# Performance work log

Hardware: AMD Instinct MI355X
Metric: run time of the kernel (lower is better)

## Reference

```python
import jax, jax.numpy as jnp
import numpy as np


def _gru(x, h, Wih, Whh, bih, bhh):
    # PyTorch GRU cell: gates ordered (reset, update, new)
    gi = x @ Wih + bih
    gh = h @ Whh + bhh
    ir, iz, inew = jnp.split(gi, 3, -1)
    hr, hz, hn = jnp.split(gh, 3, -1)
    r = jax.nn.sigmoid(ir + hr)
    u = jax.nn.sigmoid(iz + hz)
    n = jnp.tanh(inew + r * hn)
    return (1.0 - u) * n + u * h


def _kld_e(m1, s1, m2, s2):
    # elementwise term of kld_gauss (before the 0.5 * sum)
    return 2.0 * jnp.log(s2) - 2.0 * jnp.log(s1) + (s1 * s1 + (m1 - m2) ** 2) / (s2 * s2) - 1.0


def setup_inputs() -> dict:
    T, B, F, H, Z, G, A, NN, C = 32, 512, 512, 512, 256, 3, 10, 3, 1000
    key = jax.random.key(0)
    ks = iter(jax.random.split(key, 64))
    def rn(shape):
        return jax.random.normal(next(ks), shape, jnp.float32)
    def W(shape):
        return rn(shape) * (1.0 / float(np.sqrt(shape[0])))
    z = lambda n: jnp.zeros((n,), jnp.float32)
    return {
        'feat_seq': rn((T, B, F)),
        'h0': rn((B, H)),
        'eps_z': rn((T, B, Z)),
        'eps_goal': rn((G, B, Z)),
        'eps_next': rn((G, A, B, H)),
        'eps_future': rn((NN - 1, A, B, H)),
        'Wpx': W((F, H)), 'bpx': z(H),
        'Wenc1': W((2 * H, H)), 'benc1': z(H), 'Wenc2': W((H, Z)), 'benc2': z(Z),
        'Wpr1': W((H, H)), 'bpr1': z(H), 'Wpr2': W((H, Z)), 'bpr2': z(Z),
        'Wpz': W((Z, H)), 'bpz': z(H),
        'Wih1': W((2 * H, 3 * H)), 'Whh1': W((H, 3 * H)), 'bih1': z(3 * H), 'bhh1': z(3 * H),
        'Wzn': W((Z, H)), 'bzn': z(H),
        'Wprn1': W((H, H)), 'bprn1': z(H), 'Wprn2': W((H, Z)), 'bprn2': z(Z),
        'Wga': W((Z + H, H)), 'bga': z(H),
        'Woa1': W((H, H)), 'boa1': z(H), 'Woa2': W((H, Z)), 'boa2': z(Z),
        'Wna1': W((H, H)), 'bna1': z(H), 'Wna2': W((H, Z)), 'bna2': z(Z),
        'Wen': W((2 * Z, Z)), 'ben': z(Z),
        'Wact': W((H, H)), 'bact': z(H),
        'Wih2': W((2 * H, 3 * H)), 'Whh2': W((H, 3 * H)), 'bih2': z(3 * H), 'bhh2': z(3 * H),
        'Wcc': W((H, C)), 'bcc': z(C),
        'Wnc': W((H, C)), 'bnc': z(C),
    }


def reference(feat_seq, h0, eps_z, eps_goal, eps_next, eps_future,
              Wpx, bpx, Wenc1, benc1, Wenc2, benc2, Wpr1, bpr1, Wpr2, bpr2, Wpz, bpz,
              Wih1, Whh1, bih1, bhh1, Wzn, bzn, Wprn1, bprn1, Wprn2, bprn2, Wga, bga,
              Woa1, boa1, Woa2, boa2, Wna1, bna1, Wna2, bna2, Wen, ben, Wact, bact,
              Wih2, Whh2, bih2, bhh2, Wcc, bcc, Wnc, bnc):
    relu, sp = jax.nn.relu, jax.nn.softplus
    mlp2 = lambda x, W1, b1, W2, b2: relu(x @ W1 + b1) @ W2 + b2
    phi_prior = lambda x: mlp2(x, Wpr1, bpr1, Wpr2, bpr2)
    phi_prior_new = lambda x: mlp2(x, Wprn1, bprn1, Wprn2, bprn2)
    phi_next_act = lambda x: mlp2(x, Wna1, bna1, Wna2, bna2)
    phi_obs_act = lambda x: mlp2(x, Woa1, boa1, Woa2, boa2)
    phi_get_act = lambda x: relu(x @ Wga + bga)
    phi_enc_next = lambda x: relu(x @ Wen + ben)
    phi_act = lambda x: relu(x @ Wact + bact)
    G = eps_goal.shape[0]

    phix = relu(feat_seq @ Wpx + bpx)  # [T,B,H]

    def step(carry, inp):
        h, k = carry
        xp, eps = inp
        enc = mlp2(jnp.concatenate([h, xp], -1), Wenc1, benc1, Wenc2, benc2)  # enc_mean_t
        estd = sp(enc)
        pri = phi_prior(h)
        pstd = sp(pri)
        k = k + 0.5 * jnp.sum(_kld_e(enc, estd, pri, pstd))
        zt = eps * estd + enc  # reparameterized sample
        h = _gru(jnp.concatenate([xp, relu(zt @ Wpz + bpz)], -1), h, Wih1, Whh1, bih1, bhh1)
        return (h, k), None

    (h, kld_lat_goal), _ = jax.lax.scan(step, (h0, jnp.float32(0.0)), (phix, eps_z))

    obs_mean = phi_prior(h)  # [B,Z]
    obs_std = sp(obs_mean)
    obs_goal = obs_mean + eps_goal * obs_std  # [G,B,Z]
    pn_h = jnp.broadcast_to(phi_prior_new(h), (G,) + obs_mean.shape)  # [G,B,Z]
    obs_act = phi_get_act(jnp.concatenate([relu(obs_goal @ Wzn + bzn), pn_h], -1))  # [G,B,H]
    next_mean = phi_get_act(jnp.concatenate([pn_h, obs_act], -1))  # [G,B,H]
    next_std = sp(next_mean)
    next_act = next_mean[:, None] + eps_next * next_std[:, None]  # [G,A,B,H]
    pnext = phi_next_act(next_act)  # [G,A,B,Z] = prior_next_lat_goal_mean
    pnext_std = sp(pnext)
    obs_act_z = phi_obs_act(obs_act)[:, None]  # [G,1,B,Z]
    enc_next = phi_enc_next(jnp.concatenate([pnext, jnp.broadcast_to(obs_act_z, pnext.shape)], -1))
    enc_std = sp(enc_next)
    sym = 0.5 * (jnp.sum(_kld_e(obs_mean, obs_std, enc_next, enc_std), axis=(-1, -2))
                 + jnp.sum(_kld_e(enc_next, enc_std, obs_mean, obs_std), axis=(-1, -2)))  # [G,A]

    # The torch loop's `if i == 0 or ...` resets the running min for every goal
    # candidate, so only the LAST goal candidate's argmin over A survives.
    j = jnp.argmin(sym[G - 1])
    lat_goal_dis = sym[G - 1, j]
    kld_next = 0.5 * jnp.sum(_kld_e(enc_next[G - 1, j], enc_std[G - 1, j], pnext[G - 1, j], pnext_std[G - 1, j]))
    next_act_final = next_act[G - 1, j]  # [B,H]
    obs_act_final = obs_act[G - 1]       # [B,H]

    pre, cur, ha = obs_act_final, next_act_final, h
    kld_future = jnp.float32(0.0)
    future_dis = jnp.float32(0.0)
    future_finals = []
    for i in range(eps_future.shape[0]):  # next_num - 1 sequential steps
        ha = _gru(jnp.concatenate([phi_act(pre), phi_act(cur)], -1), ha, Wih2, Whh2, bih2, bhh2)
        pre = cur
        fmean = phi_get_act(jnp.concatenate([phi_prior_new(ha), pre], -1))  # [B,H]
        fstd = sp(fmean)
        fact = fmean + eps_future[i] * fstd  # [A,B,H]
        pf = phi_next_act(fact)
        pf_std = sp(pf)
        pre_z = jnp.broadcast_to(phi_next_act(pre), pf.shape)
        encf = phi_enc_next(jnp.concatenate([pf, pre_z], -1))
        encf_std = sp(encf)
        symf = 0.5 * (jnp.sum(_kld_e(obs_mean, obs_std, encf, encf_std), axis=(-1, -2))
                      + jnp.sum(_kld_e(encf, encf_std, obs_mean, obs_std), axis=(-1, -2)))  # [A]
        jj = jnp.argmin(symf)
        future_dis = future_dis + symf[jj]
        kld_future = kld_future + 0.5 * jnp.sum(_kld_e(encf[jj], encf_std[jj], pf[jj], pf_std[jj]))
        cur = fact[jj]
        future_finals.append(cur)

    out_next = next_act_final @ Wnc + bnc
    out_future = jnp.stack([out_next] + [f @ Wnc + bnc for f in future_finals], 0)  # [next_num,B,C]
    out_cur = obs_act_final @ Wcc + bcc
    return out_cur, out_future, kld_lat_goal, kld_next, lat_goal_dis, kld_future, future_dis
```

## Files before the change

kernel.cpp:

```cpp
#include <hip/hip_runtime.h>
#include <math.h>

#define DEV __device__ __forceinline__

typedef unsigned short ushort_t;
typedef __attribute__((ext_vector_type(8))) short s8v;
typedef __attribute__((ext_vector_type(4))) float f4v;

DEV float sp_(float x){ float m=fmaxf(x,0.f); return m + log1pf(expf(-fabsf(x))); }
DEV float sig_(float x){ return 1.f/(1.f+expf(-x)); }
DEV float kld_(float m1,float s1,float m2,float s2){
  float d=m1-m2;
  return 2.f*(logf(s2)-logf(s1)) + (s1*s1+d*d)/(s2*s2) - 1.f;
}
DEV unsigned short f2bf(float x){
  unsigned u = __float_as_uint(x);
  u += 0x7FFFu + ((u>>16)&1u);
  return (unsigned short)(u>>16);
}

DEV float blockReduceSum(float v){
  __shared__ float sh[8];
  #pragma unroll
  for(int o=32;o>0;o>>=1) v += __shfl_down(v,o,64);
  int lane = threadIdx.x & 63, wid = threadIdx.x >> 6;
  if(lane==0) sh[wid]=v;
  __syncthreads();
  float r = 0.f;
  if(threadIdx.x < (int)(blockDim.x>>6)) r = sh[threadIdx.x];
  if(wid==0){
    #pragma unroll
    for(int o=4;o>0;o>>=1) r += __shfl_down(r,o,64);
  }
  return r;
}

__global__ __launch_bounds__(256)
void gemm_mf(const float* __restrict__ A1, int lda1, int K1,
             const float* __restrict__ A2, int lda2, int K2,
             const ushort_t* __restrict__ BT, int ldbt,
             const float* __restrict__ bias,
             const float* __restrict__ Cadd, int rowmask, int ldcadd,
             float* __restrict__ Cm, int ldc, int N, int relu_cut)
{
  __shared__ ushort_t As[64][40];
  __shared__ ushort_t Bs[64][40];
  const int tid  = threadIdx.x;
  const int row0 = blockIdx.y * 64;
  const int col0 = blockIdx.x * 64;
  const int lane = tid & 63;
  const int w    = tid >> 6;
  const int wr   = w >> 1, wc = w & 1;
  const int Kt   = K1 + K2;
  f4v acc[2][2];
  #pragma unroll
  for(int i=0;i<2;i++){
    #pragma unroll
    for(int j=0;j<2;j++){ acc[i][j][0]=0.f; acc[i][j][1]=0.f; acc[i][j][2]=0.f; acc[i][j][3]=0.f; }
  }
  const int sr  = tid >> 2;
  const int skc = (tid & 3) * 8;

  for(int k0=0; k0<Kt; k0+=32){
    int kg = k0 + skc;
    const float* ap = (kg < K1) ? (A1 + (size_t)(row0+sr)*lda1 + kg)
                                : (A2 + (size_t)(row0+sr)*lda2 + (kg-K1));
    float4 v0 = *(const float4*)ap;
    float4 v1 = *(const float4*)(ap+4);
    s8v av;
    av[0]=(short)f2bf(v0.x); av[1]=(short)f2bf(v0.y); av[2]=(short)f2bf(v0.z); av[3]=(short)f2bf(v0.w);
    av[4]=(short)f2bf(v1.x); av[5]=(short)f2bf(v1.y); av[6]=(short)f2bf(v1.z); av[7]=(short)f2bf(v1.w);
    *(s8v*)&As[sr][skc] = av;
    int cb = col0 + sr;
    s8v bv = {0,0,0,0,0,0,0,0};
    if(cb < N) bv = *(const s8v*)(BT + (size_t)cb*ldbt + k0 + skc);
    *(s8v*)&Bs[sr][skc] = bv;
    __syncthreads();
    const int fr = lane & 15, fk = (lane >> 4) * 8;
    s8v a0 = *(const s8v*)&As[wr*32      + fr][fk];
    s8v a1 = *(const s8v*)&As[wr*32 + 16 + fr][fk];
    s8v b0 = *(const s8v*)&Bs[wc*32      + fr][fk];
    s8v b1 = *(const s8v*)&Bs[wc*32 + 16 + fr][fk];
    acc[0][0] = __builtin_amdgcn_mfma_f32_16x16x32_bf16(a0,b0,acc[0][0],0,0,0);
    acc[0][1] = __builtin_amdgcn_mfma_f32_16x16x32_bf16(a0,b1,acc[0][1],0,0,0);
    acc[1][0] = __builtin_amdgcn_mfma_f32_16x16x32_bf16(a1,b0,acc[1][0],0,0,0);
    acc[1][1] = __builtin_amdgcn_mfma_f32_16x16x32_bf16(a1,b1,acc[1][1],0,0,0);
    __syncthreads();
  }
  const int fr = lane & 15, fq = lane >> 4;
  #pragma unroll
  for(int fi=0; fi<2; fi++){
    #pragma unroll
    for(int fj=0; fj<2; fj++){
      int col = col0 + wc*32 + fj*16 + fr;
      if(col >= N) continue;
      #pragma unroll
      for(int r=0;r<4;r++){
        int row = row0 + wr*32 + fi*16 + fq*4 + r;
        float v = acc[fi][fj][r];
        if(Cadd) v += Cadd[(size_t)(row & rowmask)*ldcadd + col];
        if(bias) v += bias[col];
        if(col < relu_cut) v = fmaxf(v, 0.f);
        Cm[(size_t)row*ldc + col] = v;
      }
    }
  }
}

template<int BM>
__global__ __launch_bounds__(256)
void gemm_k(const float* __restrict__ A1, int lda1, int K1,
            const float* __restrict__ A2, int lda2, int K2,
            const float* __restrict__ Bm, int ldb,
            const float* __restrict__ bias,
            const float* __restrict__ Cadd, int rowmask, int ldcadd,
            float* __restrict__ Cm, int ldc, int N, int relu_cut)
{
  constexpr int BN = 64, BK = 32;
  constexpr int TM = BM/16;
  constexpr int PAD = (BM>=32) ? 4 : 1;
  __shared__ float As[BK][BM+PAD];
  __shared__ float Bs[BK][BN];
  const int tid = threadIdx.x;
  const int row0 = blockIdx.y * BM;
  const int col0 = blockIdx.x * BN;
  const int tx = tid & 15, ty = tid >> 4;
  float4 acc[TM];
  #pragma unroll
  for(int i=0;i<TM;i++) acc[i] = make_float4(0.f,0.f,0.f,0.f);
  const int Kt = K1 + K2;
  for(int k0=0; k0<Kt; k0+=BK){
    if constexpr (BM>=32){
      #pragma unroll
      for(int j=0;j<BM/32;j++){
        int ci = tid + j*256;
        int r  = ci >> 3;
        int kq = ci & 7;
        int kg = k0 + kq*4;
        const float* ap = (kg < K1) ? (A1 + (size_t)(row0+r)*lda1 + kg)
                                    : (A2 + (size_t)(row0+r)*lda2 + (kg-K1));
        float4 v = *(const float4*)ap;
        As[kq*4+0][r]=v.x; As[kq*4+1][r]=v.y; As[kq*4+2][r]=v.z; As[kq*4+3][r]=v.w;
      }
    } else {
      int r  = tid >> 4;
      int kq = tid & 15;
      int kg = k0 + kq*2;
      const float* ap = (kg < K1) ? (A1 + (size_t)(row0+r)*lda1 + kg)
                                  : (A2 + (size_t)(row0+r)*lda2 + (kg-K1));
      float2 v = *(const float2*)ap;
      As[kq*2+0][r]=v.x; As[kq*2+1][r]=v.y;
    }
    #pragma unroll
    for(int j=0;j<2;j++){
      int ci = tid + j*256;
      int r = ci >> 4, c4 = ci & 15;
      int c = col0 + c4*4;
      float4 v = make_float4(0.f,0.f,0.f,0.f);
      if(c < N) v = *(const float4*)(Bm + (size_t)(k0+r)*ldb + c);
      *(float4*)&Bs[r][c4*4] = v;
    }
    __syncthreads();
    #pragma unroll
    for(int kk=0; kk<BK; kk++){
      float4 b = *(const float4*)&Bs[kk][tx*4];
      if constexpr (TM==4){
        float4 a = *(const float4*)&As[kk][ty*4];
        acc[0].x=fmaf(a.x,b.x,acc[0].x); acc[0].y=fmaf(a.x,b.y,acc[0].y); acc[0].z=fmaf(a.x,b.z,acc[0].z); acc[0].w=fmaf(a.x,b.w,acc[0].w);
        acc[1].x=fmaf(a.y,b.x,acc[1].x); acc[1].y=fmaf(a.y,b.y,acc[1].y); acc[1].z=fmaf(a.y,b.z,acc[1].z); acc[1].w=fmaf(a.y,b.w,acc[1].w);
        acc[2].x=fmaf(a.z,b.x,acc[2].x); acc[2].y=fmaf(a.z,b.y,acc[2].y); acc[2].z=fmaf(a.z,b.z,acc[2].z); acc[2].w=fmaf(a.z,b.w,acc[2].w);
        acc[3].x=fmaf(a.w,b.x,acc[3].x); acc[3].y=fmaf(a.w,b.y,acc[3].y); acc[3].z=fmaf(a.w,b.z,acc[3].z); acc[3].w=fmaf(a.w,b.w,acc[3].w);
      } else if constexpr (TM==2){
        float2 a = *(const float2*)&As[kk][ty*2];
        acc[0].x=fmaf(a.x,b.x,acc[0].x); acc[0].y=fmaf(a.x,b.y,acc[0].y); acc[0].z=fmaf(a.x,b.z,acc[0].z); acc[0].w=fmaf(a.x,b.w,acc[0].w);
        acc[1].x=fmaf(a.y,b.x,acc[1].x); acc[1].y=fmaf(a.y,b.y,acc[1].y); acc[1].z=fmaf(a.y,b.z,acc[1].z); acc[1].w=fmaf(a.y,b.w,acc[1].w);
      } else {
        float a = As[kk][ty];
        acc[0].x=fmaf(a,b.x,acc[0].x); acc[0].y=fmaf(a,b.y,acc[0].y); acc[0].z=fmaf(a,b.z,acc[0].z); acc[0].w=fmaf(a,b.w,acc[0].w);
      }
    }
    __syncthreads();
  }
  int c = col0 + tx*4;
  if(c >= N) return;
  #pragma unroll
  for(int i=0;i<TM;i++){
// ... 124 lines not shown
                      float* __restrict__ h, int B_, int H_){
  int i=blockIdx.x*blockDim.x+threadIdx.x;
  if(i<B_*H_){
    int b=i/H_, c=i%H_;
    const float* gib=gi+(size_t)b*ldgi;
    const float* ghb=gh+(size_t)b*ldgh;
    float r=sig_(gib[c]+ghb[c]);
    float u=sig_(gib[H_+c]+ghb[H_+c]);
    float nn=tanhf(fmaf(r, ghb[2*H_+c], gib[2*H_+c]));
    h[i]=(1.f-u)*nn + u*h[i];
  }
}

extern "C" void kernel_launch(void* const* d_in, const int* in_sizes, int n_in,
                              void* d_out, int out_size, void* d_ws, size_t ws_size,
                              hipStream_t stream)
{
  const int T=32, B=512, F=512, H=512, Z=256, G=3, A=10, C=1000;
  const float* feat   = (const float*)d_in[0];
  const float* h0     = (const float*)d_in[1];
  const float* eps_z  = (const float*)d_in[2];
  const float* eps_g  = (const float*)d_in[3];
  const float* eps_n  = (const float*)d_in[4];
  const float* eps_f  = (const float*)d_in[5];
  const float* Wpx=(const float*)d_in[6],  *bpx=(const float*)d_in[7];
  const float* Wenc1=(const float*)d_in[8],*benc1=(const float*)d_in[9];
  const float* Wenc2=(const float*)d_in[10],*benc2=(const float*)d_in[11];
  const float* Wpr1=(const float*)d_in[12],*bpr1=(const float*)d_in[13];
  const float* Wpr2=(const float*)d_in[14],*bpr2=(const float*)d_in[15];
  const float* Wpz=(const float*)d_in[16], *bpz=(const float*)d_in[17];
  const float* Wih1=(const float*)d_in[18],*Whh1=(const float*)d_in[19];
  const float* bih1=(const float*)d_in[20],*bhh1=(const float*)d_in[21];
  const float* Wzn=(const float*)d_in[22], *bzn=(const float*)d_in[23];
  const float* Wprn1=(const float*)d_in[24],*bprn1=(const float*)d_in[25];
  const float* Wprn2=(const float*)d_in[26],*bprn2=(const float*)d_in[27];
  const float* Wga=(const float*)d_in[28], *bga=(const float*)d_in[29];
  const float* Woa1=(const float*)d_in[30],*boa1=(const float*)d_in[31];
  const float* Woa2=(const float*)d_in[32],*boa2=(const float*)d_in[33];
  const float* Wna1=(const float*)d_in[34],*bna1=(const float*)d_in[35];
  const float* Wna2=(const float*)d_in[36],*bna2=(const float*)d_in[37];
  const float* Wen=(const float*)d_in[38], *ben=(const float*)d_in[39];
  const float* Wact=(const float*)d_in[40],*bact=(const float*)d_in[41];
  const float* Wih2=(const float*)d_in[42],*Whh2=(const float*)d_in[43];
  const float* bih2=(const float*)d_in[44],*bhh2=(const float*)d_in[45];
  const float* Wcc=(const float*)d_in[46], *bcc=(const float*)d_in[47];
  const float* Wnc=(const float*)d_in[48], *bnc=(const float*)d_in[49];

  float* ws = (float*)d_ws;
  size_t off = 0;
  auto alloc = [&](size_t n){ float* p = ws + off; off += n; return p; };
  float* Hb  = alloc((size_t)B*H);
  float* E1  = alloc((size_t)B*H);
  float* P1  = alloc((size_t)B*H);
  float* ZP  = alloc((size_t)B*H);
  float* NM  = alloc((size_t)B*H);
  float* OA  = alloc((size_t)B*H);
  float* PAb = alloc((size_t)B*H);
  float* CAb = alloc((size_t)B*H);
  float* GI  = alloc((size_t)B*3*H);
  float* GH  = alloc((size_t)B*3*H);
  float* ENC = alloc((size_t)B*Z);
  float* PRI = alloc((size_t)B*Z);
  float* ZT  = alloc((size_t)B*Z);
  float* OM  = alloc((size_t)B*Z);
  float* PNH = alloc((size_t)B*Z);
  float* OAZ = alloc((size_t)B*Z);
  float* BASE= alloc((size_t)B*Z);
  float* NACT= alloc((size_t)A*B*H);
  float* PMID= alloc((size_t)A*B*H);
  float* PNX = alloc((size_t)A*B*Z);
  float* ENCN= alloc((size_t)A*B*Z);
  float* BUFA= alloc((size_t)B*H);
  float* BUFB= alloc((size_t)B*H);
  float* BUFC= alloc((size_t)B*H);
  float* C1  = alloc((size_t)B*2560);
  float* C2  = alloc((size_t)B*512);
  float* bb1 = alloc(2560);
  float* bb2 = alloc(512);
  float* SYM = alloc(16);
  float* SYMF0 = alloc(16);
  float* SYMF1 = alloc(16);
  int*   JSEL = (int*)alloc(16);
  size_t mark = off;
  auto ua = [&](size_t n){ ushort_t* p = (ushort_t*)(ws + off); off += n/2; return p; };
  ushort_t* WpxT  = ua((size_t)512*512);
  ushort_t* WB1T  = ua((size_t)2560*1024);
  ushort_t* WB2T  = ua((size_t)512*1024);
  ushort_t* WpzT  = ua((size_t)512*256);
  ushort_t* Wih1T = ua((size_t)1536*1024);
  ushort_t* Wpr1T = ua((size_t)512*512);
  ushort_t* Wpr2T = ua((size_t)256*512);
  ushort_t* Wprn1T= ua((size_t)512*512);
  ushort_t* Wprn2T= ua((size_t)256*512);
  ushort_t* WznT  = ua((size_t)512*256);
  ushort_t* WgaT  = ua((size_t)512*768);
  ushort_t* Woa1T = ua((size_t)512*512);
  ushort_t* Woa2T = ua((size_t)256*512);
  ushort_t* Wna1T = ua((size_t)512*512);
  ushort_t* Wna2T = ua((size_t)256*512);
  ushort_t* WenT  = ua((size_t)256*512);
  ushort_t* WactT = ua((size_t)512*512);
  ushort_t* Wih2T = ua((size_t)1536*1024);
  ushort_t* Whh2T = ua((size_t)1536*512);
  ushort_t* WccT  = ua((size_t)1000*512);
  ushort_t* WncT  = ua((size_t)1000*512);
  bool fast = off*4 <= ws_size;
  if(!fast) off = mark;
  size_t mark2 = off;
  float* PHIX = alloc((size_t)T*B*H);
  bool bigphix = off*4 <= ws_size;
  float* XP = nullptr;
  if(!bigphix){ off = mark2; XP = alloc((size_t)B*H); PHIX = nullptr; }

  float* outCur = (float*)d_out;
  float* outFut = outCur + (size_t)B*C;
  float* S      = outCur + (size_t)B*C*4;

  auto ew = [&](int n){ return dim3((n+255)/256); };
  auto cvt = [&](const float* W, ushort_t* WT, int K, int N){
    k_cvtT<<<(K*N+255)/256,256,0,stream>>>(W,WT,K,N);
  };
  auto mf = [&](const float* A1,int lda1,int K1,
                const float* A2,int lda2,int K2,
                const ushort_t* BT,int ldbt, const float* bias,
                const float* Cadd,int rowmask,int ldcadd,
                float* Cm,int ldc,int M,int N,int cut){
    dim3 g((N+63)/64, M/64);
    gemm_mf<<<g,256,0,stream>>>(A1,lda1,K1, A2?A2:A1,lda2,K2, BT,ldbt,bias,
                                Cadd,rowmask,ldcadd, Cm,ldc,N,cut);
  };
  auto gemm = [&](const float* A1,int lda1,int K1,
                  const float* A2,int lda2,int K2,
                  const float* Bw,int ldb, const float* bias,
                  const float* Cadd,int rowmask,int ldcadd,
                  float* Cm,int ldc,int M,int N,int relu){
    int nb = (N+63)/64;
    int cut = relu ? N : 0;
    if(M%64==0 && (M/64)*nb >= 160){
      dim3 g(nb, M/64);
      gemm_k<64><<<g,256,0,stream>>>(A1,lda1,K1, A2?A2:A1,lda2,K2, Bw,ldb,bias,
                                     Cadd,rowmask,ldcadd, Cm,ldc,N,cut);
    } else if(M%32==0 && (M/32)*nb >= 96){
      dim3 g(nb, M/32);
      gemm_k<32><<<g,256,0,stream>>>(A1,lda1,K1, A2?A2:A1,lda2,K2, Bw,ldb,bias,
                                     Cadd,rowmask,ldcadd, Cm,ldc,N,cut);
    } else {
      dim3 g(nb, M/16);
      gemm_k<16><<<g,256,0,stream>>>(A1,lda1,K1, A2?A2:A1,lda2,K2, Bw,ldb,bias,
                                     Cadd,rowmask,ldcadd, Cm,ldc,N,cut);
    }
  };

  k_init<<<1,64,0,stream>>>(S, SYM);
  k_copy<<<ew(B*H/4),256,0,stream>>>(h0, Hb, B*H/4);

  if(fast){
    cvt(Wpx, WpxT, 512, 512);
    k_packT1<<<(2560*1024+255)/256,256,0,stream>>>(Wenc1,Wpr1,Whh1,WB1T);
    k_packT2<<<(512*1024+255)/256,256,0,stream>>>(Wenc2,Wpr2,WB2T, benc1,bpr1,bhh1,bb1, benc2,bpr2,bb2);
    cvt(Wpz,  WpzT, 256, 512);
    cvt(Wih1, Wih1T,1024,1536);
    cvt(Wpr1, Wpr1T, 512, 512);
    cvt(Wpr2, Wpr2T, 512, 256);
    cvt(Wprn1,Wprn1T,512, 512);
    cvt(Wprn2,Wprn2T,512, 256);
    cvt(Wzn,  WznT,  256, 512);
    cvt(Wga,  WgaT,  768, 512);
    cvt(Woa1, Woa1T, 512, 512);
    cvt(Woa2, Woa2T, 512, 256);
    cvt(Wna1, Wna1T, 512, 512);
    cvt(Wna2, Wna2T, 512, 256);
    cvt(Wen,  WenT,  512, 256);
    cvt(Wact, WactT, 512, 512);
    cvt(Wih2, Wih2T,1024,1536);
    cvt(Whh2, Whh2T, 512,1536);
    cvt(Wcc,  WccT,  512,1000);
    cvt(Wnc,  WncT,  512,1000);

    if(bigphix)
      mf(feat,F,F, 0,0,0, WpxT,512, bpx, 0,0,0, PHIX,H, T*B,H, H);

    for(int t=0;t<T;t++){
      const float* xp;
      if(bigphix) xp = PHIX + (size_t)t*B*H;
      else { mf(feat+(size_t)t*B*F,F,F, 0,0,0, WpxT,512, bpx, 0,0,0, XP,H, B,H, H); xp = XP; }
      const float* epz = eps_z + (size_t)t*B*Z;
      mf(Hb,H,H, xp,H,H, WB1T,1024, bb1, 0,0,0, C1,2560, B,2560, 1024);
      mf(C1,2560,1024, 0,0,0, WB2T,1024, bb2, 0,0,0, C2,512, B,512, 0);
      k_kldzt<<<128,256,0,stream>>>(C2,512, C2+256,512, epz, ZT, &S[0], B, Z);
      mf(ZT,Z,Z, 0,0,0, WpzT,256, bpz, 0,0,0, ZP,H, B,H, H);
      mf(xp,H,H, ZP,H,H, Wih1T,1024, bih1, 0,0,0, GI,3*H, B,3*H, 0);
      k_gru<<<ew(B*H),256,0,stream>>>(GI,3*H, C1+1024,2560, Hb,B,H);
    }

    mf(Hb,H,H, 0,0,0, Wpr1T,512, bpr1, 0,0,0, P1,H, B,H, H);
    mf(P1,H,H, 0,0,0, Wpr2T,512, bpr2, 0,0,0, OM,Z, B,Z, 0);
    mf(Hb,H,H, 0,0,0, Wprn1T,512, bprn1, 0,0,0, P1,H, B,H, H);
    mf(P1,H,H, 0,0,0, Wprn2T,512, bprn2, 0,0,0, PNH,Z, B,Z, 0);
    k_expand<<<ew(B*Z),256,0,stream>>>(OM, eps_g+(size_t)(G-1)*B*Z, ZT, B*Z, B*Z);
    mf(ZT,Z,Z, 0,0,0, WznT,256, bzn, 0,0,0, E1,H, B,H, H);
    mf(E1,H,H, PNH,Z,Z, WgaT,768, bga, 0,0,0, OA,H, B,H, H);
    mf(PNH,Z,Z, OA,H,H, WgaT,768, bga, 0,0,0, NM,H, B,H, H);
    k_expand<<<ew(A*B*H),256,0,stream>>>(NM, eps_n+(size_t)(G-1)*A*B*H, NACT, B*H, A*B*H);
    mf(NACT,H,H, 0,0,0, Wna1T,512, bna1, 0,0,0, PMID,H, A*B,H, H);
    mf(PMID,H,H, 0,0,0, Wna2T,512, bna2, 0,0,0, PNX,Z, A*B,Z, 0);
    mf(OA,H,H, 0,0,0, Woa1T,512, boa1, 0,0,0, P1,H, B,H, H);
    mf(P1,H,H, 0,0,0, Woa2T,512, boa2, 0,0,0, OAZ,Z, B,Z, 0);
    mf(OAZ,Z,Z, 0,0,0, WenT+256,512, ben, 0,0,0, BASE,Z, B,Z, 0);
    mf(PNX,Z,Z, 0,0,0, WenT,512, 0, BASE,B-1,Z, ENCN,Z, A*B,Z, Z);
    k_sym<<<dim3(32,A),256,0,stream>>>(OM, ENCN, SYM, B*Z);
    k_argmin<<<1,64,0,stream>>>(SYM, A, &JSEL[0], &S[2], 0);
    k_kldsel<<<128,256,0,stream>>>(ENCN, PNX, &JSEL[0], B*Z, &S[1]);
    k_gather<<<ew(B*H),256,0,stream>>>(NACT, &JSEL[0], BUFA, B*H);

    const float* pre = OA; const float* cur = BUFA;
    float* futbuf[2] = {BUFB, BUFC};
    for(int i=0;i<2;i++){
      mf(pre,H,H, 0,0,0, WactT,512, bact, 0,0,0, PAb,H, B,H, H);
      mf(cur,H,H, 0,0,0, WactT,512, bact, 0,0,0, CAb,H, B,H, H);
      mf(PAb,H,H, CAb,H,H, Wih2T,1024, bih2, 0,0,0, GI,3*H, B,3*H, 0);
      mf(Hb,H,H, 0,0,0, Whh2T,512, bhh2, 0,0,0, GH,3*H, B,3*H, 0);
      k_gru<<<ew(B*H),256,0,stream>>>(GI,3*H, GH,3*H, Hb,B,H);
      pre = cur;
      mf(Hb,H,H, 0,0,0, Wprn1T,512, bprn1, 0,0,0, P1,H, B,H, H);
      mf(P1,H,H, 0,0,0, Wprn2T,512, bprn2, 0,0,0, PNH,Z, B,Z, 0);
      mf(PNH,Z,Z, pre,H,H, WgaT,768, bga, 0,0,0, NM,H, B,H, H);
      k_expand<<<ew(A*B*H),256,0,stream>>>(NM, eps_f+(size_t)i*A*B*H, NACT, B*H, A*B*H);
      mf(NACT,H,H, 0,0,0, Wna1T,512, bna1, 0,0,0, PMID,H, A*B,H, H);
      mf(PMID,H,H, 0,0,0, Wna2T,512, bna2, 0,0,0, PNX,Z, A*B,Z, 0);
      mf(pre,H,H, 0,0,0, Wna1T,512, bna1, 0,0,0, P1,H, B,H, H);
      mf(P1,H,H, 0,0,0, Wna2T,512, bna2, 0,0,0, OAZ,Z, B,Z, 0);
      mf(OAZ,Z,Z, 0,0,0, WenT+256,512, ben, 0,0,0, BASE,Z, B,Z, 0);
      mf(PNX,Z,Z, 0,0,0, WenT,512, 0, BASE,B-1,Z, ENCN,Z, A*B,Z, Z);
      float* symf = (i==0)?SYMF0:SYMF1;
      k_sym<<<dim3(32,A),256,0,stream>>>(OM, ENCN, symf, B*Z);
      k_argmin<<<1,64,0,stream>>>(symf, A, &JSEL[1+i], &S[4], 1);
      k_kldsel<<<128,256,0,stream>>>(ENCN, PNX, &JSEL[1+i], B*Z, &S[3]);
      k_gather<<<ew(B*H),256,0,stream>>>(NACT, &JSEL[1+i], futbuf[i], B*H);
      cur = futbuf[i];
    }
    mf(OA,H,H, 0,0,0, WccT,512, bcc, 0,0,0, outCur,C, B,C, 0);
    mf(BUFA,H,H, 0,0,0, WncT,512, bnc, 0,0,0, outFut,C, 3*B,C, 0);
    return;
  }

  if(bigphix)
    gemm(feat,F,F, 0,0,0, Wpx,H,bpx, 0,0,0, PHIX,H, T*B,H, 1);
  for(int t=0;t<T;t++){
    const float* xp;
    if(bigphix) xp = PHIX + (size_t)t*B*H;
    else { gemm(feat+(size_t)t*B*F,F,F, 0,0,0, Wpx,H,bpx, 0,0,0, XP,H, B,H, 1); xp = XP; }
    const float* epz = eps_z + (size_t)t*B*Z;
    gemm(Hb,H,H, xp,H,H, Wenc1,H,benc1, 0,0,0, E1,H, B,H, 1);
    gemm(E1,H,H, 0,0,0, Wenc2,Z,benc2, 0,0,0, ENC,Z, B,Z, 0);
    gemm(Hb,H,H, 0,0,0, Wpr1,H,bpr1, 0,0,0, P1,H, B,H, 1);
    gemm(P1,H,H, 0,0,0, Wpr2,Z,bpr2, 0,0,0, PRI,Z, B,Z, 0);
    k_kldzt<<<128,256,0,stream>>>(ENC,Z, PRI,Z, epz, ZT, &S[0], B, Z);
    gemm(ZT,Z,Z, 0,0,0, Wpz,H,bpz, 0,0,0, ZP,H, B,H, 1);
    gemm(xp,H,H, ZP,H,H, Wih1,3*H,bih1, 0,0,0, GI,3*H, B,3*H, 0);
    gemm(Hb,H,H, 0,0,0, Whh1,3*H,bhh1, 0,0,0, GH,3*H, B,3*H, 0);
    k_gru<<<ew(B*H),256,0,stream>>>(GI,3*H, GH,3*H, Hb,B,H);
  }
  gemm(Hb,H,H, 0,0,0, Wpr1,H,bpr1, 0,0,0, P1,H, B,H, 1);
  gemm(P1,H,H, 0,0,0, Wpr2,Z,bpr2, 0,0,0, OM,Z, B,Z, 0);
  gemm(Hb,H,H, 0,0,0, Wprn1,H,bprn1, 0,0,0, P1,H, B,H, 1);
  gemm(P1,H,H, 0,0,0, Wprn2,Z,bprn2, 0,0,0, PNH,Z, B,Z, 0);
  k_expand<<<ew(B*Z),256,0,stream>>>(OM, eps_g+(size_t)(G-1)*B*Z, ZT, B*Z, B*Z);
  gemm(ZT,Z,Z, 0,0,0, Wzn,H,bzn, 0,0,0, E1,H, B,H, 1);
  gemm(E1,H,H, PNH,Z,Z, Wga,H,bga, 0,0,0, OA,H, B,H, 1);
  gemm(PNH,Z,Z, OA,H,H, Wga,H,bga, 0,0,0, NM,H, B,H, 1);
  k_expand<<<ew(A*B*H),256,0,stream>>>(NM, eps_n+(size_t)(G-1)*A*B*H, NACT, B*H, A*B*H);
  gemm(NACT,H,H, 0,0,0, Wna1,H,bna1, 0,0,0, PMID,H, A*B,H, 1);
  gemm(PMID,H,H, 0,0,0, Wna2,Z,bna2, 0,0,0, PNX,Z, A*B,Z, 0);
  gemm(OA,H,H, 0,0,0, Woa1,H,boa1, 0,0,0, P1,H, B,H, 1);
  gemm(P1,H,H, 0,0,0, Woa2,Z,boa2, 0,0,0, OAZ,Z, B,Z, 0);
  gemm(OAZ,Z,Z, 0,0,0, Wen+(size_t)Z*Z,Z, ben, 0,0,0, BASE,Z, B,Z, 0);
  gemm(PNX,Z,Z, 0,0,0, Wen,Z, 0, BASE,B-1,Z, ENCN,Z, A*B,Z, 1);
  k_sym<<<dim3(32,A),256,0,stream>>>(OM, ENCN, SYM, B*Z);
  k_argmin<<<1,64,0,stream>>>(SYM, A, &JSEL[0], &S[2], 0);
  k_kldsel<<<128,256,0,stream>>>(ENCN, PNX, &JSEL[0], B*Z, &S[1]);
  k_gather<<<ew(B*H),256,0,stream>>>(NACT, &JSEL[0], BUFA, B*H);
  const float* pre = OA; const float* cur = BUFA;
  float* futbuf[2] = {BUFB, BUFC};
  for(int i=0;i<2;i++){
    gemm(pre,H,H, 0,0,0, Wact,H,bact, 0,0,0, PAb,H, B,H, 1);
    gemm(cur,H,H, 0,0,0, Wact,H,bact, 0,0,0, CAb,H, B,H, 1);
    gemm(PAb,H,H, CAb,H,H, Wih2,3*H,bih2, 0,0,0, GI,3*H, B,3*H, 0);
    gemm(Hb,H,H, 0,0,0, Whh2,3*H,bhh2, 0,0,0, GH,3*H, B,3*H, 0);
    k_gru<<<ew(B*H),256,0,stream>>>(GI,3*H, GH,3*H, Hb,B,H);
    pre = cur;
    gemm(Hb,H,H, 0,0,0, Wprn1,H,bprn1, 0,0,0, P1,H, B,H, 1);
    gemm(P1,H,H, 0,0,0, Wprn2,Z,bprn2, 0,0,0, PNH,Z, B,Z, 0);
    gemm(PNH,Z,Z, pre,H,H, Wga,H,bga, 0,0,0, NM,H, B,H, 1);
    k_expand<<<ew(A*B*H),256,0,stream>>>(NM, eps_f+(size_t)i*A*B*H, NACT, B*H, A*B*H);
    gemm(NACT,H,H, 0,0,0, Wna1,H,bna1, 0,0,0, PMID,H, A*B,H, 1);
    gemm(PMID,H,H, 0,0,0, Wna2,Z,bna2, 0,0,0, PNX,Z, A*B,Z, 0);
    gemm(pre,H,H, 0,0,0, Wna1,H,bna1, 0,0,0, P1,H, B,H, 1);
    gemm(P1,H,H, 0,0,0, Wna2,Z,bna2, 0,0,0, OAZ,Z, B,Z, 0);
    gemm(OAZ,Z,Z, 0,0,0, Wen+(size_t)Z*Z,Z, ben, 0,0,0, BASE,Z, B,Z, 0);
    gemm(PNX,Z,Z, 0,0,0, Wen,Z, 0, BASE,B-1,Z, ENCN,Z, A*B,Z, 1);
    float* symf = (i==0)?SYMF0:SYMF1;
    k_sym<<<dim3(32,A),256,0,stream>>>(OM, ENCN, symf, B*Z);
    k_argmin<<<1,64,0,stream>>>(symf, A, &JSEL[1+i], &S[4], 1);
    k_kldsel<<<128,256,0,stream>>>(ENCN, PNX, &JSEL[1+i], B*Z, &S[3]);
    k_gather<<<ew(B*H),256,0,stream>>>(NACT, &JSEL[1+i], futbuf[i], B*H);
    cur = futbuf[i];
  }
  gemm(OA,H,H, 0,0,0, Wcc,C,bcc, 0,0,0, outCur,C, B,C, 0);
  gemm(BUFA,H,H, 0,0,0, Wnc,C,bnc, 0,0,0, outFut,C, 3*B,C, 0);
}
```

Before: 4.376 ms.

## Hoist input projections out of recurrence, fuse KLD/reparam and GRU gates into GEMMs

Precomputes the x-dependent parts of the encoder and GRU input GEMMs for all timesteps in two large batched GEMMs, so each step only multiplies by hidden/latent inputs and adds the precomputed slice. The KLD and reparameterisation kernel is folded into the A-tile load of the Wpz GEMM, and a new gemm_gru kernel computes all three gate tiles and applies the GRU update in its epilogue, removing the separate k_kldzt and k_gru launches. The MFMA GEMM also gains double-buffered LDS with register prefetch to overlap global loads with compute. The cost is extra workspace for the precomputed buffers and more register and LDS pressure in the fused kernels.

```diff
diff --git a/kernel.cpp b/kernel.cpp
--- a/kernel.cpp
+++ b/kernel.cpp
@@ -40,11 +40,12 @@
              const float* __restrict__ A2, int lda2, int K2,
              const ushort_t* __restrict__ BT, int ldbt,
              const float* __restrict__ bias,
-             const float* __restrict__ Cadd, int rowmask, int ldcadd,
-             float* __restrict__ Cm, int ldc, int N, int relu_cut)
+             const float* __restrict__ Cadd, int rowmask, int ldcadd, int cadd_cols,
+             float* __restrict__ Cm, int ldc, int N, int relu_cut,
+             const float* __restrict__ epsP, float* __restrict__ kldS)
 {
-  __shared__ ushort_t As[64][40];
-  __shared__ ushort_t Bs[64][40];
+  __shared__ ushort_t As[2][64][40];
+  __shared__ ushort_t Bs[2][64][40];
   const int tid  = threadIdx.x;
   const int row0 = blockIdx.y * 64;
   const int col0 = blockIdx.x * 64;
@@ -52,41 +53,82 @@
   const int w    = tid >> 6;
   const int wr   = w >> 1, wc = w & 1;
   const int Kt   = K1 + K2;
+  const int nk   = Kt >> 5;
+  const int sr   = tid >> 2;
+  const int skc  = (tid & 3) * 8;
+  const bool dokld = (kldS != 0) && (blockIdx.x == 0);
+  float kloc = 0.f;
+  float fa[8];
+  s8v breg;
+
   f4v acc[2][2];
   #pragma unroll
   for(int i=0;i<2;i++){
     #pragma unroll
     for(int j=0;j<2;j++){ acc[i][j][0]=0.f; acc[i][j][1]=0.f; acc[i][j][2]=0.f; acc[i][j][3]=0.f; }
   }
-  const int sr  = tid >> 2;
-  const int skc = (tid & 3) * 8;
-
-  for(int k0=0; k0<Kt; k0+=32){
-    int kg = k0 + skc;
+
+  auto loadrg = [&](int it){
+    int kg = it*32 + skc;
     const float* ap = (kg < K1) ? (A1 + (size_t)(row0+sr)*lda1 + kg)
                                 : (A2 + (size_t)(row0+sr)*lda2 + (kg-K1));
     float4 v0 = *(const float4*)ap;
     float4 v1 = *(const float4*)(ap+4);
+    fa[0]=v0.x; fa[1]=v0.y; fa[2]=v0.z; fa[3]=v0.w;
+    fa[4]=v1.x; fa[5]=v1.y; fa[6]=v1.z; fa[7]=v1.w;
+    if(dokld){
+      const float* pp = A1 + (size_t)(row0+sr)*lda1 + K1 + kg;
+      float4 p0 = *(const float4*)pp;
+      float4 p1 = *(const float4*)(pp+4);
+      float fp[8] = {p0.x,p0.y,p0.z,p0.w,p1.x,p1.y,p1.z,p1.w};
+      #pragma unroll
+      for(int j=0;j<8;j++){
+        float m1=fa[j], m2=fp[j];
+        kloc += kld_(m1, sp_(m1), m2, sp_(m2));
+      }
+    }
+    if(epsP){
+      const float* ep = epsP + (size_t)(row0+sr)*K1 + kg;
+      #pragma unroll
+      for(int j=0;j<8;j++) fa[j] = fmaf(ep[j], sp_(fa[j]), fa[j]);
+    }
+    int cb = col0 + sr;
+    s8v bz = {0,0,0,0,0,0,0,0};
+    breg = bz;
+    if(cb < N) breg = *(const s8v*)(BT + (size_t)cb*ldbt + kg);
+  };
+  auto writeb = [&](int buf){
     s8v av;
-    av[0]=(short)f2bf(v0.x); av[1]=(short)f2bf(v0.y); av[2]=(short)f2bf(v0.z); av[3]=(short)f2bf(v0.w);
-    av[4]=(short)f2bf(v1.x); av[5]=(short)f2bf(v1.y); av[6]=(short)f2bf(v1.z); av[7]=(short)f2bf(v1.w);
-    *(s8v*)&As[sr][skc] = av;
-    int cb = col0 + sr;
-    s8v bv = {0,0,0,0,0,0,0,0};
-    if(cb < N) bv = *(const s8v*)(BT + (size_t)cb*ldbt + k0 + skc);
-    *(s8v*)&Bs[sr][skc] = bv;
-    __syncthreads();
+    #pragma unroll
+    for(int j=0;j<8;j++) av[j] = (short)f2bf(fa[j]);
+    *(s8v*)&As[buf][sr][skc] = av;
+    *(s8v*)&Bs[buf][sr][skc] = breg;
+  };
+
+  loadrg(0); writeb(0);
+  __syncthreads();
+  for(int it=0; it<nk; ++it){
+    int cur = it & 1;
+    bool more = (it+1) < nk;
+    if(more) loadrg(it+1);
     const int fr = lane & 15, fk = (lane >> 4) * 8;
-    s8v a0 = *(const s8v*)&As[wr*32      + fr][fk];
-    s8v a1 = *(const s8v*)&As[wr*32 + 16 + fr][fk];
-    s8v b0 = *(const s8v*)&Bs[wc*32      + fr][fk];
-    s8v b1 = *(const s8v*)&Bs[wc*32 + 16 + fr][fk];
+    s8v a0 = *(const s8v*)&As[cur][wr*32      + fr][fk];
+    s8v a1 = *(const s8v*)&As[cur][wr*32 + 16 + fr][fk];
+    s8v b0 = *(const s8v*)&Bs[cur][wc*32      + fr][fk];
+    s8v b1 = *(const s8v*)&Bs[cur][wc*32 + 16 + fr][fk];
     acc[0][0] = __builtin_amdgcn_mfma_f32_16x16x32_bf16(a0,b0,acc[0][0],0,0,0);
     acc[0][1] = __builtin_amdgcn_mfma_f32_16x16x32_bf16(a0,b1,acc[0][1],0,0,0);
     acc[1][0] = __builtin_amdgcn_mfma_f32_16x16x32_bf16(a1,b0,acc[1][0],0,0,0);
     acc[1][1] = __builtin_amdgcn_mfma_f32_16x16x32_bf16(a1,b1,acc[1][1],0,0,0);
+    if(more) writeb(cur^1);
     __syncthreads();
   }
+
+  if(kldS && blockIdx.x==0){
+    float tot = blockReduceSum(kloc);
+    if(tid==0) atomicAdd(kldS, 0.5f*tot);
+  }
+
   const int fr = lane & 15, fq = lane >> 4;
   #pragma unroll
   for(int fi=0; fi<2; fi++){
@@ -98,10 +140,118 @@
       for(int r=0;r<4;r++){
         int row = row0 + wr*32 + fi*16 + fq*4 + r;
         float v = acc[fi][fj][r];
-        if(Cadd) v += Cadd[(size_t)(row & rowmask)*ldcadd + col];
+        if(Cadd && col < cadd_cols) v += Cadd[(size_t)(row & rowmask)*ldcadd + col];
         if(bias) v += bias[col];
         if(col < relu_cut) v = fmaxf(v, 0.f);
         Cm[(size_t)row*ldc + col] = v;
+      }
+    }
+  }
+}
+
+__global__ __launch_bounds__(256)
+void gemm_gru(const float* __restrict__ A1, int lda1, int K1,
+              const float* __restrict__ A2, int lda2, int K2,
+              const ushort_t* __restrict__ BT, int ldbt,
+              const float* __restrict__ bias,
+              const float* __restrict__ Cadd, int ldcadd,
+              const float* __restrict__ GHp, int ldgh,
+              float* __restrict__ Hp, int Hd)
+{
+  __shared__ ushort_t As[2][64][40];
+  __shared__ ushort_t Bs[2][3][64][40];
+  const int tid  = threadIdx.x;
+  const int row0 = blockIdx.y * 64;
+  const int col0 = blockIdx.x * 64;
+  const int lane = tid & 63;
+  const int w    = tid >> 6;
+  const int wr   = w >> 1, wc = w & 1;
+  const int Kt   = K1 + K2;
+  const int nk   = Kt >> 5;
+  const int sr   = tid >> 2;
+  const int skc  = (tid & 3) * 8;
+  float fa[8];
+  s8v bregs[3];
+
+  f4v acc[3][2][2];
+  #pragma unroll
+  for(int g=0;g<3;g++){
+    #pragma unroll
+    for(int i=0;i<2;i++){
+      #pragma unroll
+      for(int j=0;j<2;j++){ acc[g][i][j][0]=0.f; acc[g][i][j][1]=0.f; acc[g][i][j][2]=0.f; acc[g][i][j][3]=0.f; }
+    }
+  }
+
+  auto loadrg = [&](int it){
+    int kg = it*32 + skc;
+    const float* ap = (kg < K1) ? (A1 + (size_t)(row0+sr)*lda1 + kg)
+                                : (A2 + (size_t)(row0+sr)*lda2 + (kg-K1));
+    float4 v0 = *(const float4*)ap;
+    float4 v1 = *(const float4*)(ap+4);
+    fa[0]=v0.x; fa[1]=v0.y; fa[2]=v0.z; fa[3]=v0.w;
+    fa[4]=v1.x; fa[5]=v1.y; fa[6]=v1.z; fa[7]=v1.w;
+    int cb = col0 + sr;
+    #pragma unroll
+    for(int g=0;g<3;g++)
+      bregs[g] = *(const s8v*)(BT + (size_t)(g*Hd + cb)*ldbt + kg);
+  };
+  auto writeb = [&](int buf){
+    s8v av;
+    #pragma unroll
+    for(int j=0;j<8;j++) av[j] = (short)f2bf(fa[j]);
+    *(s8v*)&As[buf][sr][skc] = av;
+    #pragma unroll
+    for(int g=0;g<3;g++) *(s8v*)&Bs[buf][g][sr][skc] = bregs[g];
+  };
+
+  loadrg(0); writeb(0);
+  __syncthreads();
+  for(int it=0; it<nk; ++it){
+    int cur = it & 1;
+    bool more = (it+1) < nk;
+    if(more) loadrg(it+1);
+    const int fr = lane & 15, fk = (lane >> 4) * 8;
+    s8v a0 = *(const s8v*)&As[cur][wr*32      + fr][fk];
+    s8v a1 = *(const s8v*)&As[cur][wr*32 + 16 + fr][fk];
+    #pragma unroll
+    for(int g=0;g<3;g++){
+      s8v b0 = *(const s8v*)&Bs[cur][g][wc*32      + fr][fk];
+      s8v b1 = *(const s8v*)&Bs[cur][g][wc*32 + 16 + fr][fk];
+      acc[g][0][0] = __builtin_amdgcn_mfma_f32_16x16x32_bf16(a0,b0,acc[g][0][0],0,0,0);
+      acc[g][0][1] = __builtin_amdgcn_mfma_f32_16x16x32_bf16(a0,b1,acc[g][0][1],0,0,0);
+      acc[g][1][0] = __builtin_amdgcn_mfma_f32_16x16x32_bf16(a1,b0,acc[g][1][0],0,0,0);
+      acc[g][1][1] = __builtin_amdgcn_mfma_f32_16x16x32_bf16(a1,b1,acc[g][1][1],0,0,0);
+    }
+    if(more) writeb(cur^1);
+    __syncthreads();
+  }
+
+  const int fr = lane & 15, fq = lane >> 4;
+  #pragma unroll
+  for(int fi=0; fi<2; fi++){
+    #pragma unroll
+    for(int fj=0; fj<2; fj++){
+      int col = col0 + wc*32 + fj*16 + fr;
+      #pragma unroll
+      for(int r=0;r<4;r++){
+        int row = row0 + wr*32 + fi*16 + fq*4 + r;
+        float v[3];
+        #pragma unroll
+        for(int g=0;g<3;g++){
+          float x = acc[g][fi][fj][r];
+          if(Cadd) x += Cadd[(size_t)row*ldcadd + g*Hd + col];
+          if(bias) x += bias[g*Hd + col];
+          v[g] = x;
+        }
+        const float* ghr = GHp + (size_t)row*ldgh;
+        float g0 = ghr[col], g1 = ghr[Hd+col], g2 = ghr[2*Hd+col];
+        float r_ = sig_(v[0] + g0);
+        float u_ = sig_(v[1] + g1);
+        float n_ = tanhf(fmaf(r_, g2, v[2]));
+        size_t hi = (size_t)row*Hd + col;
+        float h = Hp[hi];
+        Hp[hi] = (1.f-u_)*n_ + u_*h;
       }
     }
   }
@@ -392,7 +542,7 @@
   float* SYMF1 = alloc(16);
   int*   JSEL = (int*)alloc(16);
   size_t mark = off;
-  auto ua = [&](size_t n){ ushort_t* p = (ushort_t*)(ws + off); off += n/2; return p; };
+  auto ua = [&](size_t n){ ushort_t* p = (ushort_t*)(ws + off); off += (n+1)/2; return p; };
   ushort_t* WpxT  = ua((size_t)512*512);
   ushort_t* WB1T  = ua((size_t)2560*1024);
   ushort_t* WB2T  = ua((size_t)512*1024);
@@ -421,6 +571,11 @@
   bool bigphix = off*4 <= ws_size;
   float* XP = nullptr;
   if(!bigphix){ off = mark2; XP = alloc((size_t)B*H); PHIX = nullptr; }
+  size_t mark3 = off;
+  float* C1X = alloc((size_t)T*B*512);
+  float* GIX = alloc((size_t)T*B*1536);
+  bool bigpre = fast && bigphix && (off*4 <= ws_size);
+  if(!bigpre) off = mark3;
 
   float* outCur = (float*)d_out;
   float* outFut = outCur + (size_t)B*C;
@@ -433,11 +588,21 @@
   auto mf = [&](const float* A1,int lda1,int K1,
                 const float* A2,int lda2,int K2,
                 const ushort_t* BT,int ldbt, const float* bias,
-                const float* Cadd,int rowmask,int ldcadd,
-                float* Cm,int ldc,int M,int N,int cut){
+                const float* Cadd,int rowmask,int ldcadd,int cadd_cols,
+                float* Cm,int ldc,int M,int N,int cut,
+                const float* epsP, float* kldS){
     dim3 g((N+63)/64, M/64);
     gemm_mf<<<g,256,0,stream>>>(A1,lda1,K1, A2?A2:A1,lda2,K2, BT,ldbt,bias,
-                                Cadd,rowmask,ldcadd, Cm,ldc,N,cut);
+                                Cadd,rowmask,ldcadd,cadd_cols, Cm,ldc,N,cut, epsP,kldS);
+  };
+  auto mgru = [&](const float* A1,int lda1,int K1,
+                  const float* A2,int lda2,int K2,
+                  const ushort_t* BT,int ldbt, const float* bias,
+                  const float* Cadd,int ldcadd,
+                  const float* GHp,int ldgh, float* Hp,int M,int Hd){
+    dim3 g(Hd/64, M/64);
+    gemm_gru<<<g,256,0,stream>>>(A1,lda1,K1, A2?A2:A1,lda2,K2, BT,ldbt,bias,
+                                 Cadd,ldcadd, GHp,ldgh, Hp,Hd);
   };
   auto gemm = [&](const float* A1,int lda1,int K1,
                   const float* A2,int lda2,int K2,
@@ -488,36 +653,48 @@
     cvt(Wnc,  WncT,  512,1000);
 
     if(bigphix)
-      mf(feat,F,F, 0,0,0, WpxT,512, bpx, 0,0,0, PHIX,H, T*B,H, H);
+      mf(feat,F,F, 0,0,0, WpxT,512, bpx, 0,0,0,0, PHIX,H, T*B,H, H, 0,0);
+    if(bigpre){
+      mf(PHIX,H,H, 0,0,0, WB1T+512,1024, 0, 0,0,0,0, C1X,512, T*B,512, 0, 0,0);
+      mf(PHIX,H,H, 0,0,0, Wih1T,1024, bih1, 0,0,0,0, GIX,1536, T*B,1536, 0, 0,0);
+    }
 
     for(int t=0;t<T;t++){
       const float* xp;
       if(bigphix) xp = PHIX + (size_t)t*B*H;
-      else { mf(feat+(size_t)t*B*F,F,F, 0,0,0, WpxT,512, bpx, 0,0,0, XP,H, B,H, H); xp = XP; }
+      else { mf(feat+(size_t)t*B*F,F,F, 0,0,0, WpxT,512, bpx, 0,0,0,0, XP,H, B,H, H, 0,0); xp = XP; }
       const float* epz = eps_z + (size_t)t*B*Z;
-      mf(Hb,H,H, xp,H,H, WB1T,1024, bb1, 0,0,0, C1,2560, B,2560, 1024);
-      mf(C1,2560,1024, 0,0,0, WB2T,1024, bb2, 0,0,0, C2,512, B,512, 0);
-      k_kldzt<<<128,256,0,stream>>>(C2,512, C2+256,512, epz, ZT, &S[0], B, Z);
-      mf(ZT,Z,Z, 0,0,0, WpzT,256, bpz, 0,0,0, ZP,H, B,H, H);
-      mf(xp,H,H, ZP,H,H, Wih1T,1024, bih1, 0,0,0, GI,3*H, B,3*H, 0);
-      k_gru<<<ew(B*H),256,0,stream>>>(GI,3*H, C1+1024,2560, Hb,B,H);
-    }
-
-    mf(Hb,H,H, 0,0,0, Wpr1T,512, bpr1, 0,0,0, P1,H, B,H, H);
-    mf(P1,H,H, 0,0,0, Wpr2T,512, bpr2, 0,0,0, OM,Z, B,Z, 0);
-    mf(Hb,H,H, 0,0,0, Wprn1T,512, bprn1, 0,0,0, P1,H, B,H, H);
-    mf(P1,H,H, 0,0,0, Wprn2T,512, bprn2, 0,0,0, PNH,Z, B,Z, 0);
+      if(bigpre){
+        mf(Hb,H,H, 0,0,0, WB1T,1024, bb1,
+           C1X+(size_t)t*B*512, B-1, 512, 512, C1,2560, B,2560, 1024, 0,0);
+      } else {
+        mf(Hb,H,H, xp,H,H, WB1T,1024, bb1, 0,0,0,0, C1,2560, B,2560, 1024, 0,0);
+      }
+      mf(C1,2560,1024, 0,0,0, WB2T,1024, bb2, 0,0,0,0, C2,512, B,512, 0, 0,0);
+      mf(C2,512,256, 0,0,0, WpzT,256, bpz, 0,0,0,0, ZP,H, B,H, H, epz, &S[0]);
+      if(bigpre){
+        mgru(ZP,H,H, 0,0,0, Wih1T+512,1024, 0,
+             GIX+(size_t)t*B*1536, 1536, C1+1024, 2560, Hb, B, H);
+      } else {
+        mgru(xp,H,H, ZP,H,H, Wih1T,1024, bih1, 0,0, C1+1024, 2560, Hb, B, H);
+      }
+    }
+
+    mf(Hb,H,H, 0,0,0, Wpr1T,512, bpr1, 0,0,0,0, P1,H, B,H, H, 0,0);
+    mf(P1,H,H, 0,0,0, Wpr2T,512, bpr2, 0,0,0,0, OM,Z, B,Z, 0, 0,0);
+    mf(Hb,H,H, 0,0,0, Wprn1T,512, bprn1, 0,0,0,0, P1,H, B,H, H, 0,0);
+    mf(P1,H,H, 0,0,0, Wprn2T,512, bprn2, 0,0,0,0, PNH,Z, B,Z, 0, 0,0);
     k_expand<<<ew(B*Z),256,0,stream>>>(OM, eps_g+(size_t)(G-1)*B*Z, ZT, B*Z, B*Z);
-    mf(ZT,Z,Z, 0,0,0, WznT,256, bzn, 0,0,0, E1,H, B,H, H);
-    mf(E1,H,H, PNH,Z,Z, WgaT,768, bga, 0,0,0, OA,H, B,H, H);
-    mf(PNH,Z,Z, OA,H,H, WgaT,768, bga, 0,0,0, NM,H, B,H, H);
+    mf(ZT,Z,Z, 0,0,0, WznT,256, bzn, 0,0,0,0, E1,H, B,H, H, 0,0);
+    mf(E1,H,H, PNH,Z,Z, WgaT,768, bga, 0,0,0,0, OA,H, B,H, H, 0,0);
+    mf(PNH,Z,Z, OA,H,H, WgaT,768, bga, 0,0,0,0, NM,H, B,H, H, 0,0);
     k_expand<<<ew(A*B*H),256,0,stream>>>(NM, eps_n+(size_t)(G-1)*A*B*H, NACT, B*H, A*B*H);
-    mf(NACT,H,H, 0,0,0, Wna1T,512, bna1, 0,0,0, PMID,H, A*B,H, H);
-    mf(PMID,H,H, 0,0,0, Wna2T,512, bna2, 0,0,0, PNX,Z, A*B,Z, 0);
-    mf(OA,H,H, 0,0,0, Woa1T,512, boa1, 0,0,0, P1,H, B,H, H);
-    mf(P1,H,H, 0,0,0, Woa2T,512, boa2, 0,0,0, OAZ,Z, B,Z, 0);
-    mf(OAZ,Z,Z, 0,0,0, WenT+256,512, ben, 0,0,0, BASE,Z, B,Z, 0);
-    mf(PNX,Z,Z, 0,0,0, WenT,512, 0, BASE,B-1,Z, ENCN,Z, A*B,Z, Z);
+    mf(NACT,H,H, 0,0,0, Wna1T,512, bna1, 0,0,0,0, PMID,H, A*B,H, H, 0,0);
+    mf(PMID,H,H, 0,0,0, Wna2T,512, bna2, 0,0,0,0, PNX,Z, A*B,Z, 0, 0,0);
+    mf(OA,H,H, 0,0,0, Woa1T,512, boa1, 0,0,0,0, P1,H, B,H, H, 0,0);
+    mf(P1,H,H, 0,0,0, Woa2T,512, boa2, 0,0,0,0, OAZ,Z, B,Z, 0, 0,0);
+    mf(OAZ,Z,Z, 0,0,0, WenT+256,512, ben, 0,0,0,0, BASE,Z, B,Z, 0, 0,0);
+    mf(PNX,Z,Z, 0,0,0, WenT,512, 0, BASE,B-1,Z,Z, ENCN,Z, A*B,Z, Z, 0,0);
     k_sym<<<dim3(32,A),256,0,stream>>>(OM, ENCN, SYM, B*Z);
     k_argmin<<<1,64,0,stream>>>(SYM, A, &JSEL[0], &S[2], 0);
     k_kldsel<<<128,256,0,stream>>>(ENCN, PNX, &JSEL[0], B*Z, &S[1]);
@@ -526,22 +703,21 @@
     const float* pre = OA; const float* cur = BUFA;
     float* futbuf[2] = {BUFB, BUFC};
     for(int i=0;i<2;i++){
-      mf(pre,H,H, 0,0,0, WactT,512, bact, 0,0,0, PAb,H, B,H, H);
-      mf(cur,H,H, 0,0,0, WactT,512, bact, 0,0,0, CAb,H, B,H, H);
-      mf(PAb,H,H, CAb,H,H, Wih2T,1024, bih2, 0,0,0, GI,3*H, B,3*H, 0);
-      mf(Hb,H,H, 0,0,0, Whh2T,512, bhh2, 0,0,0, GH,3*H, B,3*H, 0);
-      k_gru<<<ew(B*H),256,0,stream>>>(GI,3*H, GH,3*H, Hb,B,H);
+      mf(pre,H,H, 0,0,0, WactT,512, bact, 0,0,0,0, PAb,H, B,H, H, 0,0);
+      mf(cur,H,H, 0,0,0, WactT,512, bact, 0,0,0,0, CAb,H, B,H, H, 0,0);
+      mf(Hb,H,H, 0,0,0, Whh2T,512, bhh2, 0,0,0,0, GH,3*H, B,3*H, 0, 0,0);
+      mgru(PAb,H,H, CAb,H,H, Wih2T,1024, bih2, 0,0, GH,3*H, Hb, B, H);
       pre = cur;
-      mf(Hb,H,H, 0,0,0, Wprn1T,512, bprn1, 0,0,0, P1,H, B,H, H);
-      mf(P1,H,H, 0,0,0, Wprn2T,512, bprn2, 0,0,0, PNH,Z, B,Z, 0);
-      mf(PNH,Z,Z, pre,H,H, WgaT,768, bga, 0,0,0, NM,H, B,H, H);
+      mf(Hb,H,H, 0,0,0, Wprn1T,512, bprn1, 0,0,0,0, P1,H, B,H, H, 0,0);
+      mf(P1,H,H, 0,0,0, Wprn2T,512, bprn2, 0,0,0,0, PNH,Z, B,Z, 0, 0,0);
+      mf(PNH,Z,Z, pre,H,H, WgaT,768, bga, 0,0,0,0, NM,H, B,H, H, 0,0);
       k_expand<<<ew(A*B*H),256,0,stream>>>(NM, eps_f+(size_t)i*A*B*H, NACT, B*H, A*B*H);
-      mf(NACT,H,H, 0,0,0, Wna1T,512, bna1, 0,0,0, PMID,H, A*B,H, H);
-      mf(PMID,H,H, 0,0,0, Wna2T,512, bna2, 0,0,0, PNX,Z, A*B,Z, 0);
-      mf(pre,H,H, 0,0,0, Wna1T,512, bna1, 0,0,0, P1,H, B,H, H);
-      mf(P1,H,H, 0,0,0, Wna2T,512, bna2, 0,0,0, OAZ,Z, B,Z, 0);
-      mf(OAZ,Z,Z, 0,0,0, WenT+256,512, ben, 0,0,0, BASE,Z, B,Z, 0);
-      mf(PNX,Z,Z, 0,0,0, WenT,512, 0, BASE,B-1,Z, ENCN,Z, A*B,Z, Z);
+      mf(NACT,H,H, 0,0,0, Wna1T,512, bna1, 0,0,0,0, PMID,H, A*B,H, H, 0,0);
+      mf(PMID,H,H, 0,0,0, Wna2T,512, bna2, 0,0,0,0, PNX,Z, A*B,Z, 0, 0,0);
+      mf(pre,H,H, 0,0,0, Wna1T,512, bna1, 0,0,0,0, P1,H, B,H, H, 0,0);
+      mf(P1,H,H, 0,0,0, Wna2T,512, bna2, 0,0,0,0, OAZ,Z, B,Z, 0, 0,0);
+      mf(OAZ,Z,Z, 0,0,0, WenT+256,512, ben, 0,0,0,0, BASE,Z, B,Z, 0, 0,0);
+      mf(PNX,Z,Z, 0,0,0, WenT,512, 0, BASE,B-1,Z,Z, ENCN,Z, A*B,Z, Z, 0,0);
       float* symf = (i==0)?SYMF0:SYMF1;
       k_sym<<<dim3(32,A),256,0,stream>>>(OM, ENCN, symf, B*Z);
       k_argmin<<<1,64,0,stream>>>(symf, A, &JSEL[1+i], &S[4], 1);
@@ -549,8 +725,8 @@
       k_gather<<<ew(B*H),256,0,stream>>>(NACT, &JSEL[1+i], futbuf[i], B*H);
       cur = futbuf[i];
     }
-    mf(OA,H,H, 0,0,0, WccT,512, bcc, 0,0,0, outCur,C, B,C, 0);
-    mf(BUFA,H,H, 0,0,0, WncT,512, bnc, 0,0,0, outFut,C, 3*B,C, 0);
+    mf(OA,H,H, 0,0,0, WccT,512, bcc, 0,0,0,0, outCur,C, B,C, 0, 0,0);
+    mf(BUFA,H,H, 0,0,0, WncT,512, bnc, 0,0,0,0, outFut,C, 3*B,C, 0, 0,0);
     return;
   }
 
```

Result: slower. 5.639 ms (+28.9%).
